# Kernel optimization log

Hardware: AMD Instinct MI355X
Metric: run time of the kernel (lower is better)

## Reference

```python
import jax, jax.numpy as jnp
import numpy as np

# Static module configuration (matches init_kwargs; img_spacing defaults to 1)
SIZE = (160, 192, 160)
SPACING = (8.0, 8.0, 8.0)
CP = tuple(int((s - 1) // sp + 4) for s, sp in zip(SIZE, SPACING))  # (23, 27, 23)


def _axis_weights_pivots(n, sp):
    """Per-axis cubic B-spline weights [n,4] and control-point indices [n,4]."""
    v = jnp.arange(n, dtype=jnp.float32) / sp
    f = jnp.floor(v)
    d = v - f  # fractional part in [0,1)
    w = jnp.stack([
        (1.0 - d) ** 3 / 6.0,                               # idx == 0
        d ** 3 / 2.0 - d ** 2 + 2.0 / 3.0,                  # idx == 1
        -d ** 3 / 2.0 + d ** 2 / 2.0 + d / 2.0 + 1.0 / 6.0, # idx == 2
        d ** 3 / 6.0,                                       # idx == 3
    ], axis=-1)  # [n, 4]
    p = f.astype(jnp.int32)[:, None] + jnp.arange(4, dtype=jnp.int32)[None, :]  # [n, 4]
    return w, p


def setup_inputs() -> dict:
    key = jax.random.key(0)
    mesh = jax.random.normal(key, (4, 3, *CP), dtype=jnp.float32)
    return {"mesh": mesh}


def reference(mesh):
    # Separable tensor-product form of the 4^3-offset gather-MAC loop:
    # flow[b,c,x,y,z] = sum_{a,b2,c2} wX[x,a]*wY[y,b2]*wZ[z,c2]
    #                    * mesh[b,c, fX[x]+a, fY[y]+b2, fZ[z]+c2]
    wx, px = _axis_weights_pivots(SIZE[0], SPACING[0])
    wy, py = _axis_weights_pivots(SIZE[1], SPACING[1])
    wz, pz = _axis_weights_pivots(SIZE[2], SPACING[2])
    # gather+contract along x: [B,C,X,4,CY,CZ] x [X,4] -> [B,C,X,CY,CZ]
    t = jnp.einsum('bcxakl,xa->bcxkl', mesh[:, :, px, :, :], wx)
    # gather+contract along y: [B,C,X,Y,4,CZ] x [Y,4] -> [B,C,X,Y,CZ]
    t = jnp.einsum('bcxyal,ya->bcxyl', t[:, :, :, py, :], wy)
    # gather+contract along z: [B,C,X,Y,Z,4] x [Z,4] -> [B,C,X,Y,Z]
    flow = jnp.einsum('bcxyza,za->bcxyz', t[:, :, :, :, pz], wz)
    return flow
```

## Files before the change

kernel.cpp:

```cpp
#include <hip/hip_runtime.h>


#define SPX 160
#define SPY 192
#define SPZ 160
#define CPX 23
#define CPY 27
#define CPZ 23

#define TXS  32
#define TXYS 72

__global__ __launch_bounds__(256, 8) void ffd_kernel(const float* __restrict__ mesh,
                                                     float* __restrict__ out) {
    const int yb  = blockIdx.x;
    const int xb  = blockIdx.y;
    const int bc  = blockIdx.z;
    const int tid = threadIdx.x;

    __shared__ __align__(16) float wlds[8][4];
    __shared__ __align__(16) float tX[CPZ * TXS];
    __shared__ __align__(16) float tXY[CPZ * TXYS];

    if (tid < 32) {
        int j = tid >> 2, a = tid & 3;
        float d  = (float)j * 0.125f;
        float d2 = d * d, d3 = d2 * d;
        float w;
        if (a == 0)      { float e = 1.0f - d; w = e * e * e * (1.0f / 6.0f); }
        else if (a == 1) { w = 0.5f * d3 - d2 + (2.0f / 3.0f); }
        else if (a == 2) { w = -0.5f * d3 + 0.5f * d2 + 0.5f * d + (1.0f / 6.0f); }
        else             { w = d3 * (1.0f / 6.0f); }
        wlds[j][a] = w;
    }
    __syncthreads();

    const float* mbase = mesh + (size_t)bc * (CPX * CPY * CPZ)
                              + (size_t)xb * (CPY * CPZ) + (size_t)yb * CPZ;
    #pragma unroll
    for (int j = 0; j < 3; ++j) {
        int i = tid + 256 * j;
        if (j < 2 || tid < 736 - 512) {
            int b2 = i & 3, x8 = (i >> 2) & 7, cz = i >> 5;
            const float* mp = mbase + b2 * CPZ + cz;
            float acc = wlds[x8][0] * mp[0]
                      + wlds[x8][1] * mp[CPY * CPZ]
                      + wlds[x8][2] * mp[2 * CPY * CPZ]
                      + wlds[x8][3] * mp[3 * CPY * CPZ];
            tX[cz * TXS + x8 * 4 + b2] = acc;
        }
    }
    __syncthreads();

    #pragma unroll
    for (int j = 0; j < 6; ++j) {
        int i = tid + 256 * j;
        if (j < 5 || tid < 1472 - 1280) {
            int y8 = i & 7, x8 = (i >> 3) & 7, cz = i >> 6;
            const float4 t4 = *(const float4*)&tX[cz * TXS + x8 * 4];
            float acc = wlds[y8][0] * t4.x + wlds[y8][1] * t4.y
                      + wlds[y8][2] * t4.z + wlds[y8][3] * t4.w;
            tXY[cz * TXYS + x8 * 8 + y8] = acc;
        }
    }
    __syncthreads();

    const int zt = tid & 7;
    const int h  = zt & 1;
    const int qo = zt >> 1;
    const float4 Wr0 = *(const float4*)&wlds[4 * h + 0][0];
    const float4 Wr1 = *(const float4*)&wlds[4 * h + 1][0];
    const float4 Wr2 = *(const float4*)&wlds[4 * h + 2][0];
    const float4 Wr3 = *(const float4*)&wlds[4 * h + 3][0];

    float* oblk = out + ((size_t)bc * SPX * SPY
                       + (size_t)(xb * 8) * SPY
                       + (size_t)(yb * 8)) * SPZ;
    #pragma unroll
    for (int pass = 0; pass < 2; ++pass) {
        int row = pass * 32 + (tid >> 3);
        int x8 = row >> 3, y8 = row & 7;
        const float* tcol = &tXY[x8 * 8 + y8];
        float* orow = oblk + ((size_t)x8 * SPY + (size_t)y8) * SPZ;
        #pragma unroll
        for (int k = 0; k < 5; ++k) {
            int qa = 4 * k + qo;
            float m0 = tcol[qa * TXYS];
            float m1 = tcol[(qa + 1) * TXYS];
            float m2 = tcol[(qa + 2) * TXYS];
            float m3 = tcol[(qa + 3) * TXYS];
            float4 o;
            o.x = Wr0.x * m0 + Wr0.y * m1 + Wr0.z * m2 + Wr0.w * m3;
            o.y = Wr1.x * m0 + Wr1.y * m1 + Wr1.z * m2 + Wr1.w * m3;
            o.z = Wr2.x * m0 + Wr2.y * m1 + Wr2.z * m2 + Wr2.w * m3;
            o.w = Wr3.x * m0 + Wr3.y * m1 + Wr3.z * m2 + Wr3.w * m3;
            *(float4*)&orow[32 * k + 4 * zt] = o;
        }
    }
}

extern "C" void kernel_launch(void* const* d_in, const int* in_sizes, int n_in,
                              void* d_out, int out_size, void* d_ws, size_t ws_size,
                              hipStream_t stream) {
    const float* mesh = (const float*)d_in[0];
    float* out = (float*)d_out;
    dim3 grid(SPY / 8, SPX / 8, 4 * 3);
    ffd_kernel<<<grid, 256, 0, stream>>>(mesh, out);
}
```

Baseline: 41.92 us.

## Partition FFD block work per wavefront and replace barriers with waitcnt

Each 64-lane wavefront now owns two x-slices and carries all three separable contraction stages in its own LDS region. The three __syncthreads barriers become s_waitcnt lgkmcnt(0), which removes block-wide synchronization. The LDS intermediate layout also moves to per-wave arrays so the z-stage reads contiguous values instead of strided columns. Each wave now recomputes its own x-contraction, and the weight table is written by every wave. Cross-lane visibility within a wave relies only on waitcnt without a barrier, which is a correctness risk.

```diff
diff --git a/kernel.cpp b/kernel.cpp
--- a/kernel.cpp
+++ b/kernel.cpp
@@ -7,23 +7,25 @@
 #define CPX 23
 #define CPY 27
 #define CPZ 23
+#define MXS (CPY * CPZ)
 
-#define TXS  32
-#define TXYS 72
+#define WAVE_LDS_SYNC() asm volatile("s_waitcnt lgkmcnt(0)" ::: "memory")
 
 __global__ __launch_bounds__(256, 8) void ffd_kernel(const float* __restrict__ mesh,
                                                      float* __restrict__ out) {
-    const int yb  = blockIdx.x;
-    const int xb  = blockIdx.y;
-    const int bc  = blockIdx.z;
-    const int tid = threadIdx.x;
+    const int yb   = blockIdx.x;
+    const int xb   = blockIdx.y;
+    const int bc   = blockIdx.z;
+    const int tid  = threadIdx.x;
+    const int lane = tid & 63;
+    const int wid  = tid >> 6;
 
     __shared__ __align__(16) float wlds[8][4];
-    __shared__ __align__(16) float tX[CPZ * TXS];
-    __shared__ __align__(16) float tXY[CPZ * TXYS];
+    __shared__ __align__(16) float tXw[4][2][24][4];
+    __shared__ __align__(16) float tXYw[4][2][8][24];
 
-    if (tid < 32) {
-        int j = tid >> 2, a = tid & 3;
+    if (lane < 32) {
+        int j = lane >> 2, a = lane & 3;
         float d  = (float)j * 0.125f;
         float d2 = d * d, d3 = d2 * d;
         float w;
@@ -33,39 +35,41 @@
         else             { w = d3 * (1.0f / 6.0f); }
         wlds[j][a] = w;
     }
-    __syncthreads();
+    WAVE_LDS_SYNC();
 
     const float* mbase = mesh + (size_t)bc * (CPX * CPY * CPZ)
-                              + (size_t)xb * (CPY * CPZ) + (size_t)yb * CPZ;
+                              + (size_t)xb * MXS + (size_t)yb * CPZ;
     #pragma unroll
     for (int j = 0; j < 3; ++j) {
-        int i = tid + 256 * j;
-        if (j < 2 || tid < 736 - 512) {
-            int b2 = i & 3, x8 = (i >> 2) & 7, cz = i >> 5;
+        int i = lane + 64 * j;
+        if (j < 2 || lane < 184 - 128) {
+            int b2 = i & 3, xh = (i >> 2) & 1, cz = i >> 3;
+            const float4 wr = *(const float4*)&wlds[2 * wid + xh][0];
             const float* mp = mbase + b2 * CPZ + cz;
-            float acc = wlds[x8][0] * mp[0]
-                      + wlds[x8][1] * mp[CPY * CPZ]
-                      + wlds[x8][2] * mp[2 * CPY * CPZ]
-                      + wlds[x8][3] * mp[3 * CPY * CPZ];
-            tX[cz * TXS + x8 * 4 + b2] = acc;
+            float acc = wr.x * mp[0]
+                      + wr.y * mp[MXS]
+                      + wr.z * mp[2 * MXS]
+                      + wr.w * mp[3 * MXS];
+            tXw[wid][xh][cz][b2] = acc;
         }
     }
-    __syncthreads();
+    WAVE_LDS_SYNC();
 
     #pragma unroll
     for (int j = 0; j < 6; ++j) {
-        int i = tid + 256 * j;
-        if (j < 5 || tid < 1472 - 1280) {
-            int y8 = i & 7, x8 = (i >> 3) & 7, cz = i >> 6;
-            const float4 t4 = *(const float4*)&tX[cz * TXS + x8 * 4];
-            float acc = wlds[y8][0] * t4.x + wlds[y8][1] * t4.y
-                      + wlds[y8][2] * t4.z + wlds[y8][3] * t4.w;
-            tXY[cz * TXYS + x8 * 8 + y8] = acc;
+        int i = lane + 64 * j;
+        if (j < 5 || lane < 368 - 320) {
+            int y8 = i & 7, xh = (i >> 3) & 1, cz = i >> 4;
+            const float4 wr = *(const float4*)&wlds[y8][0];
+            const float4 t4 = *(const float4*)&tXw[wid][xh][cz][0];
+            tXYw[wid][xh][y8][cz] = wr.x * t4.x + wr.y * t4.y
+                                  + wr.z * t4.z + wr.w * t4.w;
         }
     }
-    __syncthreads();
+    WAVE_LDS_SYNC();
 
-    const int zt = tid & 7;
+    const int zt = lane & 7;
+    const int y8 = lane >> 3;
     const int h  = zt & 1;
     const int qo = zt >> 1;
     const float4 Wr0 = *(const float4*)&wlds[4 * h + 0][0];
@@ -77,18 +81,17 @@
                        + (size_t)(xb * 8) * SPY
                        + (size_t)(yb * 8)) * SPZ;
     #pragma unroll
-    for (int pass = 0; pass < 2; ++pass) {
-        int row = pass * 32 + (tid >> 3);
-        int x8 = row >> 3, y8 = row & 7;
-        const float* tcol = &tXY[x8 * 8 + y8];
+    for (int xh = 0; xh < 2; ++xh) {
+        int x8 = 2 * wid + xh;
+        const float* tcol = &tXYw[wid][xh][y8][0];
         float* orow = oblk + ((size_t)x8 * SPY + (size_t)y8) * SPZ;
         #pragma unroll
         for (int k = 0; k < 5; ++k) {
             int qa = 4 * k + qo;
-            float m0 = tcol[qa * TXYS];
-            float m1 = tcol[(qa + 1) * TXYS];
-            float m2 = tcol[(qa + 2) * TXYS];
-            float m3 = tcol[(qa + 3) * TXYS];
+            float m0 = tcol[qa];
+            float m1 = tcol[qa + 1];
+            float m2 = tcol[qa + 2];
+            float m3 = tcol[qa + 3];
             float4 o;
             o.x = Wr0.x * m0 + Wr0.y * m1 + Wr0.z * m2 + Wr0.w * m3;
             o.y = Wr1.x * m0 + Wr1.y * m1 + Wr1.z * m2 + Wr1.w * m3;
```

Measured after the change: 41.56 us. No clear change (-0.9%).
